# Kernel optimization log

Hardware: AMD Instinct MI355X
Metric: run time of the kernel (lower is better)

Reference implementation:

```python
import jax, jax.numpy as jnp
import numpy as np

TWO_PI = 2.0 * np.pi


def _kernel_mean(X, Z, ksize):
    # Pairwise squared distances via the expanded form (same math as
    # sum((X[:,None,:]-Z)**2, -1), without the N x N x D intermediate).
    x2 = jnp.sum(X * X, axis=-1)            # [N]
    z2 = jnp.sum(Z * Z, axis=-1)            # [M]
    d2 = x2[:, None] + z2[None, :] - 2.0 * (X @ Z.T)  # [N, M]
    G = jnp.exp(-d2 / ksize) / jnp.sqrt(TWO_PI * ksize)
    return jnp.mean(G)


def setup_inputs() -> dict:
    key = jax.random.key(0)
    kx, kz = jax.random.split(key)
    N, D = 8192, 3
    x = jax.random.normal(kx, (N, D), dtype=jnp.float32)
    # flag == 'sp': Z = spherical(shape) = standard normal, ndim=3
    z = jax.random.normal(kz, (N, D), dtype=jnp.float32)
    ks = jnp.float32(1.0)
    theta = jnp.float32(1.0)
    return {"x": x, "z": z, "ks": ks, "theta": theta}


def reference(x, z, ks, theta):
    mxx = _kernel_mean(x, x, ks)
    mzz = _kernel_mean(z, z, ks)
    mxz = _kernel_mean(x, z, ks)
    r = jnp.log(jnp.sqrt(mxx * mzz + 1e-5) / (mxz + 1e-5))
    # Layer returns (inputs, Z, r*theta); r*theta is also the added loss.
    return (x, z, r * theta)
```

## Files before the change

### kernel.cpp

```cpp
#include <hip/hip_runtime.h>
#include <math.h>

#define NPTS 8192
#define TPB 256
#define IPT 2
#define ISPAN (TPB * IPT)
#define ICH (NPTS / ISPAN)
#define JTILE 128
#define JCH (NPTS / JTILE)
#define NBLK (ICH * JCH)

static __device__ __forceinline__ float fexp2(float v) {
    return __builtin_amdgcn_exp2f(v);
}

__global__ __launch_bounds__(TPB) void itl_pairwise_kernel(
    const float* __restrict__ x, const float* __restrict__ z,
    const float* __restrict__ ks_p, float* __restrict__ partials,
    float* __restrict__ out)
{
    __shared__ float4 xs[JTILE];
    __shared__ float4 zs[JTILE];
    __shared__ float red[3][TPB / 64];

    const int t = threadIdx.x;
    const int ib = (blockIdx.x & (ICH - 1)) * ISPAN;
    const int jb = (blockIdx.x / ICH) * JTILE;

    const float c2 = 1.44269504088896340736f / ks_p[0];
    const float c1 = 2.0f * c2;

    if (t < 12) {
        const int k = blockIdx.x * 12 + t;
        const float4* src = (k < 6144) ? ((const float4*)x + k)
                                       : ((const float4*)z + (k - 6144));
        ((float4*)out)[k] = *src;
    }

    if (t < JTILE) {
        const int j = jb + t;
        const float a0 = x[3 * j], a1 = x[3 * j + 1], a2 = x[3 * j + 2];
        xs[t] = make_float4(a0 * c1, a1 * c1, a2 * c1,
                            fexp2(-(a0 * a0 + a1 * a1 + a2 * a2) * c2));
    } else {
        const int j = jb + (t - JTILE);
        const float b0 = z[3 * j], b1 = z[3 * j + 1], b2 = z[3 * j + 2];
        zs[t - JTILE] = make_float4(b0 * c1, b1 * c1, b2 * c1,
                                    fexp2(-(b0 * b0 + b1 * b1 + b2 * b2) * c2));
    }

    const int i0 = ib + t, i1 = ib + t + TPB;
    const float x00 = x[3 * i0], x01 = x[3 * i0 + 1], x02 = x[3 * i0 + 2];
    const float x10 = x[3 * i1], x11 = x[3 * i1 + 1], x12 = x[3 * i1 + 2];
    const float z00 = z[3 * i0], z01 = z[3 * i0 + 1], z02 = z[3 * i0 + 2];
    const float z10 = z[3 * i1], z11 = z[3 * i1 + 1], z12 = z[3 * i1 + 2];
    const float ex0 = fexp2(-(x00 * x00 + x01 * x01 + x02 * x02) * c2);
    const float ex1 = fexp2(-(x10 * x10 + x11 * x11 + x12 * x12) * c2);
    const float ez0 = fexp2(-(z00 * z00 + z01 * z01 + z02 * z02) * c2);
    const float ez1 = fexp2(-(z10 * z10 + z11 * z11 + z12 * z12) * c2);

    __syncthreads();

    float sxx0 = 0.f, sxx1 = 0.f, szz0 = 0.f, szz1 = 0.f, sxz0 = 0.f, sxz1 = 0.f;
#pragma unroll 8
    for (int jj = 0; jj < JTILE; ++jj) {
        const float4 a = xs[jj];
        const float4 b = zs[jj];
        sxx0 += a.w * fexp2(x00 * a.x + x01 * a.y + x02 * a.z);
        sxx1 += a.w * fexp2(x10 * a.x + x11 * a.y + x12 * a.z);
        szz0 += b.w * fexp2(z00 * b.x + z01 * b.y + z02 * b.z);
        szz1 += b.w * fexp2(z10 * b.x + z11 * b.y + z12 * b.z);
        sxz0 += b.w * fexp2(x00 * b.x + x01 * b.y + x02 * b.z);
        sxz1 += b.w * fexp2(x10 * b.x + x11 * b.y + x12 * b.z);
    }

    float sxx = sxx0 * ex0 + sxx1 * ex1;
    float szz = szz0 * ez0 + szz1 * ez1;
    float sxz = sxz0 * ex0 + sxz1 * ex1;

    for (int off = 32; off; off >>= 1) {
        sxx += __shfl_down(sxx, off);
        szz += __shfl_down(szz, off);
        sxz += __shfl_down(sxz, off);
    }
    const int lane = t & 63, wv = t >> 6;
    if (lane == 0) { red[0][wv] = sxx; red[1][wv] = szz; red[2][wv] = sxz; }
    __syncthreads();
    if (t == 0) {
        partials[blockIdx.x]            = red[0][0] + red[0][1] + red[0][2] + red[0][3];
        partials[NBLK + blockIdx.x]     = red[1][0] + red[1][1] + red[1][2] + red[1][3];
        partials[2 * NBLK + blockIdx.x] = red[2][0] + red[2][1] + red[2][2] + red[2][3];
    }
}

__global__ __launch_bounds__(TPB) void itl_finalize_kernel(
    const float* __restrict__ partials, const float* __restrict__ ks_p,
    const float* __restrict__ theta_p, float* __restrict__ out_scalar)
{
    __shared__ float red[3][TPB / 64];
    const int t = threadIdx.x;
    float s[3];
#pragma unroll
    for (int k = 0; k < 3; ++k) {
        float v = 0.f;
        for (int b = t; b < NBLK; b += TPB) v += partials[k * NBLK + b];
        for (int off = 32; off; off >>= 1) v += __shfl_down(v, off);
        s[k] = v;
    }
    if ((t & 63) == 0) {
        red[0][t >> 6] = s[0]; red[1][t >> 6] = s[1]; red[2][t >> 6] = s[2];
    }
    __syncthreads();
    if (t == 0) {
        const double inv = 1.0 / ((double)NPTS * (double)NPTS);
        const double scale = 1.0 / sqrt(2.0 * M_PI * (double)ks_p[0]);
        const double mxx = (double)(red[0][0] + red[0][1] + red[0][2] + red[0][3]) * inv * scale;
        const double mzz = (double)(red[1][0] + red[1][1] + red[1][2] + red[1][3]) * inv * scale;
        const double mxz = (double)(red[2][0] + red[2][1] + red[2][2] + red[2][3]) * inv * scale;
        const double r = log(sqrt(mxx * mzz + 1e-5) / (mxz + 1e-5));
        out_scalar[0] = (float)(r * (double)theta_p[0]);
    }
}

extern "C" void kernel_launch(void* const* d_in, const int* in_sizes, int n_in,
                              void* d_out, int out_size, void* d_ws, size_t ws_size,
                              hipStream_t stream) {
    const float* x     = (const float*)d_in[0];
    const float* z     = (const float*)d_in[1];
    const float* ks    = (const float*)d_in[2];
    const float* theta = (const float*)d_in[3];
    float* out      = (float*)d_out;
    float* partials = (float*)d_ws;

    itl_pairwise_kernel<<<NBLK, TPB, 0, stream>>>(x, z, ks, partials, out);
    itl_finalize_kernel<<<1, TPB, 0, stream>>>(partials, ks, theta, out + NPTS * 3 * 2);
}
```

Before: 101.5 us.

## Exploit symmetry of self-kernel matrices by computing only upper-triangular tiles

Splits the work into separate block types: full tiles for the cross (x,z) matrix and upper-triangular tiles for the xx and zz matrices. The diagonal is added analytically as N, and off-diagonal sums are doubled in the finalize step. Each thread now handles 4 rows against a single j-tile instead of 2 rows against three matrices. The goal is to remove almost half the exp work for the symmetric terms. In exchange, diagonal band blocks carry predicated masking and a small loop to map block index to tile.

```diff
diff --git a/kernel.cpp b/kernel.cpp
--- a/kernel.cpp
+++ b/kernel.cpp
@@ -3,12 +3,15 @@
 
 #define NPTS 8192
 #define TPB 256
-#define IPT 2
+#define IPT 4
 #define ISPAN (TPB * IPT)
-#define ICH (NPTS / ISPAN)
+#define NSTRIP (NPTS / ISPAN)
 #define JTILE 128
-#define JCH (NPTS / JTILE)
-#define NBLK (ICH * JCH)
+#define JT_TOTAL (NPTS / JTILE)
+#define BPS (ISPAN / JTILE)
+#define NXZ (NSTRIP * JT_TOTAL)
+#define NTRI 288
+#define NBLK (NXZ + 2 * NTRI)
 
 static __device__ __forceinline__ float fexp2(float v) {
     return __builtin_amdgcn_exp2f(v);
@@ -19,78 +22,88 @@
     const float* __restrict__ ks_p, float* __restrict__ partials,
     float* __restrict__ out)
 {
-    __shared__ float4 xs[JTILE];
-    __shared__ float4 zs[JTILE];
-    __shared__ float red[3][TPB / 64];
+    __shared__ float4 js[JTILE];
+    __shared__ float red[TPB / 64];
 
     const int t = threadIdx.x;
-    const int ib = (blockIdx.x & (ICH - 1)) * ISPAN;
-    const int jb = (blockIdx.x / ICH) * JTILE;
+    const int b = blockIdx.x;
+
+    int mat, s = 0, jt;
+    bool band;
+    if (b < NXZ) {
+        mat = 0; s = b >> 6; jt = b & 63; band = false;
+    } else {
+        int r = b - NXZ;
+        mat = (r < NTRI) ? 1 : 2;
+        if (mat == 2) r -= NTRI;
+        while (r >= JT_TOTAL - BPS * s) { r -= JT_TOTAL - BPS * s; ++s; }
+        jt = BPS * s + r;
+        band = (r < BPS);
+    }
+    const int ib = s * ISPAN;
+    const int jb = jt * JTILE;
 
     const float c2 = 1.44269504088896340736f / ks_p[0];
     const float c1 = 2.0f * c2;
 
     if (t < 12) {
-        const int k = blockIdx.x * 12 + t;
-        const float4* src = (k < 6144) ? ((const float4*)x + k)
-                                       : ((const float4*)z + (k - 6144));
-        ((float4*)out)[k] = *src;
+        const int k = b * 12 + t;
+        if (k < 12288) {
+            const float4* src = (k < 6144) ? ((const float4*)x + k)
+                                           : ((const float4*)z + (k - 6144));
+            ((float4*)out)[k] = *src;
+        }
     }
+
+    const float* __restrict__ isrc = (mat == 2) ? z : x;
+    const float* __restrict__ jsrc = (mat == 1) ? x : z;
 
     if (t < JTILE) {
         const int j = jb + t;
-        const float a0 = x[3 * j], a1 = x[3 * j + 1], a2 = x[3 * j + 2];
-        xs[t] = make_float4(a0 * c1, a1 * c1, a2 * c1,
+        const float a0 = jsrc[3 * j], a1 = jsrc[3 * j + 1], a2 = jsrc[3 * j + 2];
+        js[t] = make_float4(a0 * c1, a1 * c1, a2 * c1,
                             fexp2(-(a0 * a0 + a1 * a1 + a2 * a2) * c2));
-    } else {
-        const int j = jb + (t - JTILE);
-        const float b0 = z[3 * j], b1 = z[3 * j + 1], b2 = z[3 * j + 2];
-        zs[t - JTILE] = make_float4(b0 * c1, b1 * c1, b2 * c1,
-                                    fexp2(-(b0 * b0 + b1 * b1 + b2 * b2) * c2));
     }
 
-    const int i0 = ib + t, i1 = ib + t + TPB;
-    const float x00 = x[3 * i0], x01 = x[3 * i0 + 1], x02 = x[3 * i0 + 2];
-    const float x10 = x[3 * i1], x11 = x[3 * i1 + 1], x12 = x[3 * i1 + 2];
-    const float z00 = z[3 * i0], z01 = z[3 * i0 + 1], z02 = z[3 * i0 + 2];
-    const float z10 = z[3 * i1], z11 = z[3 * i1 + 1], z12 = z[3 * i1 + 2];
-    const float ex0 = fexp2(-(x00 * x00 + x01 * x01 + x02 * x02) * c2);
-    const float ex1 = fexp2(-(x10 * x10 + x11 * x11 + x12 * x12) * c2);
-    const float ez0 = fexp2(-(z00 * z00 + z01 * z01 + z02 * z02) * c2);
-    const float ez1 = fexp2(-(z10 * z10 + z11 * z11 + z12 * z12) * c2);
+    float p0[IPT], p1[IPT], p2[IPT], ef[IPT];
+    int iv[IPT];
+#pragma unroll
+    for (int k = 0; k < IPT; ++k) {
+        const int i = ib + t + k * TPB;
+        iv[k] = i;
+        p0[k] = isrc[3 * i]; p1[k] = isrc[3 * i + 1]; p2[k] = isrc[3 * i + 2];
+        ef[k] = fexp2(-(p0[k] * p0[k] + p1[k] * p1[k] + p2[k] * p2[k]) * c2);
+    }
 
     __syncthreads();
 
-    float sxx0 = 0.f, sxx1 = 0.f, szz0 = 0.f, szz1 = 0.f, sxz0 = 0.f, sxz1 = 0.f;
+    float acc[IPT] = {0.f, 0.f, 0.f, 0.f};
+    if (!band) {
 #pragma unroll 8
-    for (int jj = 0; jj < JTILE; ++jj) {
-        const float4 a = xs[jj];
-        const float4 b = zs[jj];
-        sxx0 += a.w * fexp2(x00 * a.x + x01 * a.y + x02 * a.z);
-        sxx1 += a.w * fexp2(x10 * a.x + x11 * a.y + x12 * a.z);
-        szz0 += b.w * fexp2(z00 * b.x + z01 * b.y + z02 * b.z);
-        szz1 += b.w * fexp2(z10 * b.x + z11 * b.y + z12 * b.z);
-        sxz0 += b.w * fexp2(x00 * b.x + x01 * b.y + x02 * b.z);
-        sxz1 += b.w * fexp2(x10 * b.x + x11 * b.y + x12 * b.z);
+        for (int jj = 0; jj < JTILE; ++jj) {
+            const float4 a = js[jj];
+#pragma unroll
+            for (int k = 0; k < IPT; ++k)
+                acc[k] += a.w * fexp2(p0[k] * a.x + p1[k] * a.y + p2[k] * a.z);
+        }
+    } else {
+#pragma unroll 4
+        for (int jj = 0; jj < JTILE; ++jj) {
+            const float4 a = js[jj];
+            const int j = jb + jj;
+#pragma unroll
+            for (int k = 0; k < IPT; ++k) {
+                const float v = a.w * fexp2(p0[k] * a.x + p1[k] * a.y + p2[k] * a.z);
+                acc[k] += (j > iv[k]) ? v : 0.0f;
+            }
+        }
     }
 
-    float sxx = sxx0 * ex0 + sxx1 * ex1;
-    float szz = szz0 * ez0 + szz1 * ez1;
-    float sxz = sxz0 * ex0 + sxz1 * ex1;
-
-    for (int off = 32; off; off >>= 1) {
-        sxx += __shfl_down(sxx, off);
-        szz += __shfl_down(szz, off);
-        sxz += __shfl_down(sxz, off);
-    }
-    const int lane = t & 63, wv = t >> 6;
-    if (lane == 0) { red[0][wv] = sxx; red[1][wv] = szz; red[2][wv] = sxz; }
+    float ssum = acc[0] * ef[0] + acc[1] * ef[1] + acc[2] * ef[2] + acc[3] * ef[3];
+    for (int off = 32; off; off >>= 1) ssum += __shfl_down(ssum, off);
+    if ((t & 63) == 0) red[t >> 6] = ssum;
     __syncthreads();
-    if (t == 0) {
-        partials[blockIdx.x]            = red[0][0] + red[0][1] + red[0][2] + red[0][3];
-        partials[NBLK + blockIdx.x]     = red[1][0] + red[1][1] + red[1][2] + red[1][3];
-        partials[2 * NBLK + blockIdx.x] = red[2][0] + red[2][1] + red[2][2] + red[2][3];
-    }
+    if (t == 0) partials[b] = red[0] + red[1] + red[2] + red[3];
 }
 
 __global__ __launch_bounds__(TPB) void itl_finalize_kernel(
@@ -99,24 +112,28 @@
 {
     __shared__ float red[3][TPB / 64];
     const int t = threadIdx.x;
-    float s[3];
-#pragma unroll
-    for (int k = 0; k < 3; ++k) {
-        float v = 0.f;
-        for (int b = t; b < NBLK; b += TPB) v += partials[k * NBLK + b];
-        for (int off = 32; off; off >>= 1) v += __shfl_down(v, off);
-        s[k] = v;
+    float v0 = 0.f, v1 = 0.f, v2 = 0.f;
+    for (int i = t; i < NXZ; i += TPB) v0 += partials[i];
+    for (int i = t; i < NTRI; i += TPB) v1 += partials[NXZ + i];
+    for (int i = t; i < NTRI; i += TPB) v2 += partials[NXZ + NTRI + i];
+    for (int off = 32; off; off >>= 1) {
+        v0 += __shfl_down(v0, off);
+        v1 += __shfl_down(v1, off);
+        v2 += __shfl_down(v2, off);
     }
     if ((t & 63) == 0) {
-        red[0][t >> 6] = s[0]; red[1][t >> 6] = s[1]; red[2][t >> 6] = s[2];
+        red[0][t >> 6] = v0; red[1][t >> 6] = v1; red[2][t >> 6] = v2;
     }
     __syncthreads();
     if (t == 0) {
+        const double Sxz = (double)(red[0][0] + red[0][1] + red[0][2] + red[0][3]);
+        const double Sxx = 2.0 * (double)(red[1][0] + red[1][1] + red[1][2] + red[1][3]) + (double)NPTS;
+        const double Szz = 2.0 * (double)(red[2][0] + red[2][1] + red[2][2] + red[2][3]) + (double)NPTS;
         const double inv = 1.0 / ((double)NPTS * (double)NPTS);
         const double scale = 1.0 / sqrt(2.0 * M_PI * (double)ks_p[0]);
-        const double mxx = (double)(red[0][0] + red[0][1] + red[0][2] + red[0][3]) * inv * scale;
-        const double mzz = (double)(red[1][0] + red[1][1] + red[1][2] + red[1][3]) * inv * scale;
-        const double mxz = (double)(red[2][0] + red[2][1] + red[2][2] + red[2][3]) * inv * scale;
+        const double mxx = Sxx * inv * scale;
+        const double mzz = Szz * inv * scale;
+        const double mxz = Sxz * inv * scale;
         const double r = log(sqrt(mxx * mzz + 1e-5) / (mxz + 1e-5));
         out_scalar[0] = (float)(r * (double)theta_p[0]);
     }
```

New measurement: 97.72 us. -3.7%, faster.
